# Performance work log

Measured on AMD Instinct MI355X. Metric: run time of the kernel, lower is better.

Reference implementation:

```python
import jax, jax.numpy as jnp
import numpy as np

C, DI, N, K, R = 64, 128, 16, 4, 4   # d_model, d_inner, d_state, d_conv, dt_rank
B, H, W = 4, 96, 96


def _layer_params(key):
    ks = jax.random.split(key, 6)
    p = {}
    p['ln_g'] = jnp.ones((C,), jnp.float32)
    p['ln_b'] = jnp.zeros((C,), jnp.float32)
    p['in_w'] = jax.random.normal(ks[0], (2 * DI, C), jnp.float32) / np.sqrt(C)
    p['conv_w'] = jax.random.normal(ks[1], (DI, K), jnp.float32) / np.sqrt(K)
    p['conv_b'] = jnp.zeros((DI,), jnp.float32)
    p['xp_w'] = jax.random.normal(ks[2], (R + 2 * N, DI), jnp.float32) / np.sqrt(DI)
    p['dt_w'] = jax.random.normal(ks[3], (DI, R), jnp.float32) / np.sqrt(R)
    p['dt_b'] = jnp.full((DI,), -4.0, jnp.float32)  # softplus(-4) ~ 0.018, sane dt
    p['A_log'] = jnp.broadcast_to(jnp.log(jnp.arange(1, N + 1, dtype=jnp.float32)), (DI, N)) + jnp.zeros((DI, N), jnp.float32)
    p['D'] = jnp.ones((DI,), jnp.float32)
    p['out_w'] = jax.random.normal(ks[4], (C, DI), jnp.float32) / np.sqrt(DI)
    p['skip'] = jnp.ones((1,), jnp.float32)
    p['pr_w'] = jax.random.normal(ks[5], (C, C), jnp.float32) / np.sqrt(C)
    p['pr_b'] = jnp.zeros((C,), jnp.float32)
    return p


def setup_inputs() -> dict:
    key = jax.random.key(0)
    k0, k1, k2 = jax.random.split(key, 3)
    inp = {'x': jax.random.normal(k0, (B, C, H, W), jnp.float32)}
    for i, k in ((1, k1), (2, k2)):
        for n, v in _layer_params(k).items():
            inp[f'{n}{i}'] = v
    return inp


def _silu(x):
    return x * jax.nn.sigmoid(x)


def _layer_norm(x, g, b, eps=1e-5):
    m = x.mean(-1, keepdims=True)
    v = x.var(-1, keepdims=True)
    return (x - m) * jax.lax.rsqrt(v + eps) * g + b


def _instance_norm(x, eps=1e-5):  # x: [B, C, H, W], no affine
    m = x.mean((2, 3), keepdims=True)
    v = x.var((2, 3), keepdims=True)
    return (x - m) * jax.lax.rsqrt(v + eps)


def _causal_conv(x, w, b):  # x: [B, L, D]; w: [D, K] depthwise; causal pad left
    L = x.shape[1]
    xp = jnp.pad(x, ((0, 0), (K - 1, 0), (0, 0)))
    y = b
    for k in range(K):
        y = y + xp[:, k:k + L, :] * w[:, k]
    return y


def _mamba(x, in_w, conv_w, conv_b, xp_w, dt_w, dt_b, A_log, Dp, out_w):
    # x: [B, L, C]
    xz = x @ in_w.T                       # [B, L, 2*DI]
    xin, z = jnp.split(xz, 2, axis=-1)
    xc = _silu(_causal_conv(xin, conv_w, conv_b))   # [B, L, DI]
    dbl = xc @ xp_w.T                     # [B, L, R + 2N]
    dt, Bm, Cm = jnp.split(dbl, [R, R + N], axis=-1)
    dt = jax.nn.softplus(dt @ dt_w.T + dt_b)        # [B, L, DI]
    A = -jnp.exp(A_log)                   # [DI, N]
    a = jnp.exp(dt[..., None] * A)                        # [B, L, DI, N]
    bb = dt[..., None] * Bm[:, :, None, :] * xc[..., None]  # [B, L, DI, N]

    def comb(l, r):
        a1, b1 = l
        a2, b2 = r
        return (a1 * a2, a2 * b1 + b2)

    _, h = jax.lax.associative_scan(comb, (a, bb), axis=1)  # h: [B, L, DI, N]
    y = jnp.einsum('bldn,bln->bld', h, Cm) + Dp * xc
    y = y * _silu(z)
    return y @ out_w.T                    # [B, L, C]


def _mamba_layer(x4, p):
    # x4: [B, C, H, W]
    b, c, h, w = x4.shape
    xf = x4.reshape(b, c, h * w).transpose(0, 2, 1)   # [B, L, C]
    xn = _layer_norm(xf, p['ln_g'], p['ln_b'])
    xm = _mamba(xn, p['in_w'], p['conv_w'], p['conv_b'], p['xp_w'], p['dt_w'],
                p['dt_b'], p['A_log'], p['D'], p['out_w']) + p['skip'] * xf
    xm = xm @ p['pr_w'].T + p['pr_b']
    return xm.transpose(0, 2, 1).reshape(b, c, h, w)


_PNAMES = ['ln_g', 'ln_b', 'in_w', 'conv_w', 'conv_b', 'xp_w', 'dt_w', 'dt_b',
           'A_log', 'D', 'out_w', 'skip', 'pr_w', 'pr_b']


def _forward(x, *ps):
    p1 = dict(zip(_PNAMES, ps[:14]))
    p2 = dict(zip(_PNAMES, ps[14:]))
    identity = x
    h = jax.nn.relu(_instance_norm(x))
    h = _mamba_layer(h, p1)
    h = jax.nn.relu(_instance_norm(h))
    h = _mamba_layer(h, p2)
    return h + identity


def reference(x, ln_g1, ln_b1, in_w1, conv_w1, conv_b1, xp_w1, dt_w1, dt_b1,
              A_log1, D1, out_w1, skip1, pr_w1, pr_b1,
              ln_g2, ln_b2, in_w2, conv_w2, conv_b2, xp_w2, dt_w2, dt_b2,
              A_log2, D2, out_w2, skip2, pr_w2, pr_b2):
    return _forward(x, ln_g1, ln_b1, in_w1, conv_w1, conv_b1, xp_w1, dt_w1, dt_b1,
                    A_log1, D1, out_w1, skip1, pr_w1, pr_b1,
                    ln_g2, ln_b2, in_w2, conv_w2, conv_b2, xp_w2, dt_w2, dt_b2,
                    A_log2, D2, out_w2, skip2, pr_w2, pr_b2)
```

## Files before the change

kernel.cpp:

```cpp
#include <hip/hip_runtime.h>
#include <math.h>

#define BB 4
#define CC 64
#define DI 128
#define NS 16
#define LL 9216
#define NT (LL / 64)

#define GCH 576
#define LCH 16
#define NSEQ 8192
#define SD  512
#define NG 24
#define GS 24

typedef __attribute__((ext_vector_type(8))) short bf16x8;
typedef __attribute__((ext_vector_type(4))) float fx4;
#define MFMA16 __builtin_amdgcn_mfma_f32_16x16x32_bf16

static __device__ __forceinline__ unsigned short f2b(float f) {
  unsigned u = __float_as_uint(f);
  u += 0x7fffu + ((u >> 16) & 1u);
  return (unsigned short)(u >> 16);
}
static __device__ __forceinline__ float b2f(unsigned short s) {
  return __uint_as_float(((unsigned)s) << 16);
}
static __device__ __forceinline__ float silu_f(float x) {
  return x / (1.f + __expf(-x));
}

static __device__ __forceinline__ void powers16(float e1, float* a) {
  float p2 = e1 * e1, p4 = p2 * p2, p8 = p4 * p4;
  a[0] = e1;      a[1] = p2;      a[2] = p2 * e1;      a[3] = p4;
  a[4] = p4 * e1; a[5] = p4 * p2; a[6] = p4 * p2 * e1; a[7] = p8;
  a[8] = p8 * e1; a[9] = p8 * p2; a[10] = p8 * p2 * e1; a[11] = p8 * p4;
  a[12] = p8 * p4 * e1; a[13] = p8 * p4 * p2; a[14] = p8 * p4 * p2 * e1; a[15] = p8 * p8;
}

static __device__ __forceinline__ float dt_and_a(float v, float A0, bool aone, bool afast,
                                                 const float* __restrict__ Alog, int d,
                                                 float* a) {
  float em = __expf(-fabsf(v));
  float t = 1.f + em;
  float dtv = fmaxf(v, 0.f) + __logf(t);
  if (aone) {
    float e1 = ((v >= 0.f) ? em : 1.f) / t;
    powers16(e1, a);
  } else if (afast) {
    powers16(__expf(dtv * A0), a);
  } else {
    #pragma unroll
    for (int n = 0; n < 16; ++n) a[n] = __expf(dtv * -__expf(Alog[d * NS + n]));
  }
  return dtv;
}

__global__ __launch_bounds__(256) void k_cvt(const float* __restrict__ inw1, const float* __restrict__ xpw1,
                                             const float* __restrict__ ow1, const float* __restrict__ pw1,
                                             const float* __restrict__ inw2, const float* __restrict__ xpw2,
                                             const float* __restrict__ ow2, const float* __restrict__ pw2,
                                             unsigned short* __restrict__ wb) {
  int idx = blockIdx.x * 256 + threadIdx.x;
  int layer = idx >= 34816;
  int e = idx - layer * 34816;
  const float* inw = layer ? inw2 : inw1;
  const float* xpw = layer ? xpw2 : xpw1;
  const float* ow = layer ? ow2 : ow1;
  const float* pw = layer ? pw2 : pw1;
  float v;
  if (e < 16384) v = inw[e];
  else if (e < 22528) { int t = e - 16384; int r = t >> 7, c = t & 127; v = (r < 36) ? xpw[r * 128 + c] : 0.f; }
  else if (e < 30720) v = ow[e - 22528];
  else v = pw[e - 30720];
  wb[idx] = f2b(v);
}

__global__ __launch_bounds__(256) void k_stats(const float* __restrict__ p,
                                               float* __restrict__ stats) {
  int bc = blockIdx.x;
  const float* row = p + (size_t)bc * LL;
  float s = 0.f, s2 = 0.f;
  for (int i = threadIdx.x; i < LL; i += 256) {
    float v = row[i];
    s += v; s2 += v * v;
  }
  #pragma unroll
  for (int o = 32; o > 0; o >>= 1) {
    s += __shfl_down(s, o);
    s2 += __shfl_down(s2, o);
  }
  __shared__ float red[8];
  int w = threadIdx.x >> 6;
  if ((threadIdx.x & 63) == 0) { red[w] = s; red[4 + w] = s2; }
  __syncthreads();
  if (threadIdx.x == 0) {
    float S = red[0] + red[1] + red[2] + red[3];
    float S2 = red[4] + red[5] + red[6] + red[7];
    float m = S * (1.f / LL);
    float var = S2 * (1.f / LL) - m * m;
    stats[bc * 2] = m;
    stats[bc * 2 + 1] = rsqrtf(var + 1e-5f);
  }
}

__global__ __launch_bounds__(256) void k_fusein(const float* __restrict__ p,
                                                const float* __restrict__ stats,
                                                const float* __restrict__ g,
                                                const float* __restrict__ be,
                                                const unsigned short* __restrict__ w_b,
                                                float* __restrict__ xf,
                                                unsigned short* __restrict__ xin_b,
                                                unsigned short* __restrict__ sz_b) {
  int b = blockIdx.x / NT;
  int l0 = (blockIdx.x % NT) * 64;
  __shared__ float T[64][65];
  __shared__ unsigned short Tb[64][72];
  int li = threadIdx.x & 63;
  int c0 = threadIdx.x >> 6;
  #pragma unroll
  for (int j = 0; j < 16; ++j) {
    int c = c0 * 16 + j;
    float m = stats[(b * CC + c) * 2];
    float rs = stats[(b * CC + c) * 2 + 1];
    float v = p[((size_t)(b * CC + c)) * LL + l0 + li];
    T[li][c] = fmaxf((v - m) * rs, 0.f);
  }
  __syncthreads();
  int lane = threadIdx.x & 63;
  int w = threadIdx.x >> 6;
  float gv = g[lane], bv = be[lane];
  for (int j = 0; j < 16; ++j) {
    int row = w * 16 + j;
    float v = T[row][lane];
    float s = v, s2 = v * v;
    #pragma unroll
    for (int o = 32; o > 0; o >>= 1) { s += __shfl_xor(s, o); s2 += __shfl_xor(s2, o); }
    float m = s * (1.f / 64.f);
    float var = s2 * (1.f / 64.f) - m * m;
    float rs = rsqrtf(var + 1e-5f);
    size_t off = ((size_t)b * LL + l0 + row) * CC + lane;
    xf[off] = v;
    Tb[row][lane] = f2b((v - m) * rs * gv + bv);
  }
  __syncthreads();
  int wv = threadIdx.x >> 6;
  int lr = lane & 15, kg = lane >> 4;
  int m0 = wv * 16;
  int rowg0 = blockIdx.x * 64 + m0;
  bf16x8 a0 = *(const bf16x8*)&Tb[m0 + lr][kg * 8];
  bf16x8 a1 = *(const bf16x8*)&Tb[m0 + lr][32 + kg * 8];
  #pragma unroll
  for (int nt = 0; nt < 16; ++nt) {
    bf16x8 b0 = *(const bf16x8*)&w_b[(size_t)(nt * 16 + lr) * CC + kg * 8];
    bf16x8 b1 = *(const bf16x8*)&w_b[(size_t)(nt * 16 + lr) * CC + 32 + kg * 8];
    fx4 c = {0.f, 0.f, 0.f, 0.f};
    c = MFMA16(a0, b0, c, 0, 0, 0);
    c = MFMA16(a1, b1, c, 0, 0, 0);
    #pragma unroll
    for (int r = 0; r < 4; ++r) {
      int row = rowg0 + kg * 4 + r, col = nt * 16 + lr;
      if (col < 128) xin_b[(size_t)row * DI + col] = f2b(c[r]);
      else           sz_b[(size_t)row * DI + col - 128] = f2b(silu_f(c[r]));
    }
  }
}

__global__ __launch_bounds__(128) void k_scanAX(const unsigned short* __restrict__ xin_b,
                                                const float* __restrict__ cw,
                                                const float* __restrict__ cb,
                                                const unsigned short* __restrict__ xpw_b,
                                                const float* __restrict__ Alog,
                                                const float* __restrict__ dtw,
                                                const float* __restrict__ dtbp,
                                                float* __restrict__ dbl,
                                                unsigned short* __restrict__ xc_b,
                                                float* __restrict__ dts,
                                                float* __restrict__ hl) {
  int g = blockIdx.x % GCH;
  int b = blockIdx.x / GCH;
  __shared__ float dblP[2][16][40];
  __shared__ unsigned short xcS[16][136];
  int wv = threadIdx.x >> 6, lane = threadIdx.x & 63;
  int lr = lane & 15, kg = lane >> 4;
  {
    int lloc = g * LCH + lr;
    size_t row = (size_t)b * LL + lloc;
    const bf16x8 zv8 = {0, 0, 0, 0, 0, 0, 0, 0};
    fx4 acc[3];
    #pragma unroll
    for (int nt = 0; nt < 3; ++nt) acc[nt] = (fx4){0.f, 0.f, 0.f, 0.f};
    #pragma unroll
    for (int kk = 0; kk < 2; ++kk) {
      int cbase = (wv * 2 + kk) * 32 + kg * 8;
      bf16x8 x3 = *(const bf16x8*)&xin_b[row * DI + cbase];
      bf16x8 x2 = (lloc >= 1) ? *(const bf16x8*)&xin_b[(row - 1) * DI + cbase] : zv8;
      bf16x8 x1 = (lloc >= 2) ? *(const bf16x8*)&xin_b[(row - 2) * DI + cbase] : zv8;
      bf16x8 x0 = (lloc >= 3) ? *(const bf16x8*)&xin_b[(row - 3) * DI + cbase] : zv8;
      bf16x8 a;
      #pragma unroll
      for (int e = 0; e < 8; ++e) {
        int dd = cbase + e;
        float4 w4 = *(const float4*)&cw[dd * 4];
        float v = cb[dd] + b2f((unsigned short)x0[e]) * w4.x + b2f((unsigned short)x1[e]) * w4.y
                + b2f((unsigned short)x2[e]) * w4.z + b2f((unsigned short)x3[e]) * w4.w;
        a[e] = (short)f2b(silu_f(v));
      }
      *(bf16x8*)&xcS[lr][cbase] = a;
      #pragma unroll
      for (int nt = 0; nt < 3; ++nt) {
        bf16x8 bfr = *(const bf16x8*)&xpw_b[(size_t)(nt * 16 + lr) * DI + cbase];
        acc[nt] = MFMA16(a, bfr, acc[nt], 0, 0, 0);
      }
    }
    #pragma unroll
    for (int nt = 0; nt < 3; ++nt)
      #pragma unroll
      for (int r = 0; r < 4; ++r) {
        int col = nt * 16 + lr;
        if (col < 36) dblP[wv][kg * 4 + r][col] = acc[nt][r];
      }
  }
  __syncthreads();
  {
    size_t dbase = ((size_t)b * LL + g * LCH) * 36;
    for (int e = threadIdx.x; e < 576; e += 128) {
      int r = e / 36, c = e - r * 36;
      float v = dblP[0][r][c] + dblP[1][r][c];
      dblP[0][r][c] = v;
      dbl[dbase + e] = v;
    }
    size_t xbase = ((size_t)b * LL + g * LCH) * DI;
    #pragma unroll
    for (int j = 0; j < 2; ++j) {
      int c = threadIdx.x + 128 * j;
      int row = c >> 4, col = (c & 15) * 8;
      *(bf16x8*)&xc_b[xbase + row * DI + col] = *(const bf16x8*)&xcS[row][col];
    }
  }
  __syncthreads();
  int d = threadIdx.x;
  float A0 = -__expf(Alog[d * NS]);
  bool afast = true;
  #pragma unroll
  for (int n = 1; n < 16; ++n) {
    float An = -__expf(Alog[d * NS + n]);
    afast = afast && (fabsf(An - A0 * (float)(n + 1)) <= 1e-3f * (float)(n + 1) * fabsf(A0));
  }
  bool aone = afast && (A0 == -1.0f);
  float4 w4 = *(const float4*)&dtw[d * 4];
  float dtbv = dtbp[d];
  float h[16];
  #pragma unroll
  for (int n = 0; n < 16; ++n) h[n] = 0.f;
  float dtsum = 0.f;
  #pragma unroll 4
  for (int l = 0; l < LCH; ++l) {
    float xcv = b2f(xcS[l][d]);
    float4 qv = *(float4*)&dblP[0][l][0];
    float v = dtbv + qv.x * w4.x + qv.y * w4.y + qv.z * w4.z + qv.w * w4.w;
    float a[16];
    float dtv = dt_and_a(v, A0, aone, afast, Alog, d, a);
    float dx = dtv * xcv;
    dtsum += dtv;
    float4 b0 = *(float4*)&dblP[0][l][4];
    float4 b1 = *(float4*)&dblP[0][l][8];
    float4 b2 = *(float4*)&dblP[0][l][12];
    float4 b3 = *(float4*)&dblP[0][l][16];
    h[0]  = a[0]  * h[0]  + dx * b0.x;  h[1]  = a[1]  * h[1]  + dx * b0.y;
    h[2]  = a[2]  * h[2]  + dx * b0.z;  h[3]  = a[3]  * h[3]  + dx * b0.w;
    h[4]  = a[4]  * h[4]  + dx * b1.x;  h[5]  = a[5]  * h[5]  + dx * b1.y;
    h[6]  = a[6]  * h[6]  + dx * b1.z;  h[7]  = a[7]  * h[7]  + dx * b1.w;
    h[8]  = a[8]  * h[8]  + dx * b2.x;  h[9]  = a[9]  * h[9]  + dx * b2.y;
    h[10] = a[10] * h[10] + dx * b2.z;  h[11] = a[11] * h[11] + dx * b2.w;
    h[12] = a[12] * h[12] + dx * b3.x;  h[13] = a[13] * h[13] + dx * b3.y;
    h[14] = a[14] * h[14] + dx * b3.z;  h[15] = a[15] * h[15] + dx * b3.w;
  }
  dts[(size_t)g * SD + b * DI + d] = dtsum;
  size_t o = (size_t)g * NSEQ + ((size_t)b * DI + d) * NS;
  #pragma unroll
  for (int j = 0; j < 4; ++j)
    *(float4*)&hl[o + j * 4] = make_float4(h[j * 4], h[j * 4 + 1], h[j * 4 + 2], h[j * 4 + 3]);
}

__global__ __launch_bounds__(256) void k_scan2a(const float* __restrict__ dts,
                                                const float* __restrict__ hl,
                                                const float* __restrict__ Alog,
                                                float* __restrict__ gap,
                                                float* __restrict__ ghl) {
  int t = blockIdx.x * 256 + threadIdx.x;
  int grp = t >> 13, seq = t & (NSEQ - 1);
  int sd = seq >> 4;
  float An = -__expf(Alog[seq & (DI * NS - 1)]);
  float A = 1.f, H = 0.f;
  int c0 = grp * GS;
  #pragma unroll 4
  for (int c = 0; c < GS; ++c) {
    float a = __expf(An * dts[(size_t)(c0 + c) * SD + sd]);
    H = a * H + hl[(size_t)(c0 + c) * NSEQ + seq];
    A *= a;
  }
  gap[t] = A;
  ghl[t] = H;
}

__global__ __launch_bounds__(256) void k_scan2bc(const float* __restrict__ dts,
                                                 const float* __restrict__ hl,
                                                 const float* __restrict__ gap,
                                                 const float* __restrict__ ghl,
                                                 const float* __restrict__ Alog,
                                                 float* __restrict__ hi) {
  int t = blockIdx.x * 256 + threadIdx.x;
  int grp = t >> 13, seq = t & (NSEQ - 1);
  int sd = seq >> 4;
  float An = -__expf(Alog[seq & (DI * NS - 1)]);
  float h = 0.f;
  for (int gg = 0; gg < grp; ++gg)
    h = gap[gg * NSEQ + seq] * h + ghl[gg * NSEQ + seq];
  int c0 = grp * GS;
  #pragma unroll 4
  for (int c = 0; c < GS; ++c) {
    float a = __expf(An * dts[(size_t)(c0 + c) * SD + sd]);
    hi[(size_t)(c0 + c) * NSEQ + seq] = h;
    h = a * h + hl[(size_t)(c0 + c) * NSEQ + seq];
  }
}

__global__ __launch_bounds__(128) void k_scanCO(const float* __restrict__ dbl,
                                                const unsigned short* __restrict__ xc_b,
                                                const unsigned short* __restrict__ sz_b,
                                                const float* __restrict__ Alog,
                                                const float* __restrict__ dtw,
                                                const float* __restrict__ dtbp,
                                                const float* __restrict__ Dp,
                                                const float* __restrict__ hi,
                                                const unsigned short* __restrict__ ow_b,
                                                const float* __restrict__ xf,
                                                const float* __restrict__ skipv,
                                                const unsigned short* __restrict__ pw_b,
                                                const float* __restrict__ pb,
                                                const float* __restrict__ ident,
                                                float* __restrict__ dst, int addid) {
  int g = blockIdx.x % GCH;
  int b = blockIdx.x / GCH;
  int d = threadIdx.x;
  __shared__ float Bms[LCH * NS];
  __shared__ float Cms[LCH * NS];
  __shared__ float Dts[LCH][4];
  __shared__ unsigned short xcS[16][136];
  __shared__ unsigned short yS[16][136];
  __shared__ unsigned short tmpS[16][72];
  {
    int tid = threadIdx.x;
    size_t rb0 = ((size_t)b * LL + g * LCH) * 36;
    if (tid < 64) {
      int l = tid >> 2, n4 = (tid & 3) * 4;
      *(float4*)&Bms[l * 16 + n4] = *(const float4*)&dbl[rb0 + (size_t)l * 36 + 4 + n4];
    } else {
      int l = (tid - 64) >> 2, n4 = (tid & 3) * 4;
      *(float4*)&Cms[l * 16 + n4] = *(const float4*)&dbl[rb0 + (size_t)l * 36 + 20 + n4];
    }
    if (tid < 16)
      *(float4*)&Dts[tid][0] = *(const float4*)&dbl[rb0 + (size_t)tid * 36];
    size_t xbase = ((size_t)b * LL + g * LCH) * DI;
    #pragma unroll
    for (int j = 0; j < 2; ++j) {
      int c = tid + 128 * j;
      int row = c >> 4, col = (c & 15) * 8;
      *(bf16x8*)&xcS[row][col] = *(const bf16x8*)&xc_b[xbase + row * DI + col];
    }
  }
  float A0 = -__expf(Alog[d * NS]);
  bool afast = true;
  #pragma unroll
  for (int n = 1; n < 16; ++n) {
    float An = -__expf(Alog[d * NS + n]);
    afast = afast && (fabsf(An - A0 * (float)(n + 1)) <= 1e-3f * (float)(n + 1) * fabsf(A0));
  }
  bool aone = afast && (A0 == -1.0f);
  float4 w4 = *(const float4*)&dtw[d * 4];
  float dtbv = dtbp[d];
  float Dv = Dp[d];
  __syncthreads();
  size_t o = (size_t)g * NSEQ + ((size_t)b * DI + d) * NS;
  float h[16];
  #pragma unroll
  for (int j = 0; j < 4; ++j) {
    float4 hv = *(const float4*)&hi[o + j * 4];
    h[j * 4 + 0] = hv.x; h[j * 4 + 1] = hv.y; h[j * 4 + 2] = hv.z; h[j * 4 + 3] = hv.w;
  }
  size_t base = ((size_t)b * LL + g * LCH) * DI + d;
  #pragma unroll 4
  for (int l = 0; l < LCH; ++l) {
    float xcv = b2f(xcS[l][d]);
    float sg = b2f(sz_b[base + (size_t)l * DI]);
    float4 qv = *(float4*)&Dts[l][0];
    float v = dtbv + qv.x * w4.x + qv.y * w4.y + qv.z * w4.z + qv.w * w4.w;
    float a[16];
    float dtv = dt_and_a(v, A0, aone, afast, Alog, d, a);
    float4 b0 = *(float4*)&Bms[l * 16];
    float4 b1 = *(float4*)&Bms[l * 16 + 4];
    float4 b2 = *(float4*)&Bms[l * 16 + 8];
    float4 b3 = *(float4*)&Bms[l * 16 + 12];
    float4 c0 = *(float4*)&Cms[l * 16];
    float4 c1 = *(float4*)&Cms[l * 16 + 4];
    float4 c2 = *(float4*)&Cms[l * 16 + 8];
    float4 c3 = *(float4*)&Cms[l * 16 + 12];
    float dx = dtv * xcv;
    float yv = Dv * xcv;
    h[0]  = a[0]  * h[0]  + dx * b0.x;  yv += h[0]  * c0.x;
    h[1]  = a[1]  * h[1]  + dx * b0.y;  yv += h[1]  * c0.y;
    h[2]  = a[2]  * h[2]  + dx * b0.z;  yv += h[2]  * c0.z;
    h[3]  = a[3]  * h[3]  + dx * b0.w;  yv += h[3]  * c0.w;
    h[4]  = a[4]  * h[4]  + dx * b1.x;  yv += h[4]  * c1.x;
    h[5]  = a[5]  * h[5]  + dx * b1.y;  yv += h[5]  * c1.y;
    h[6]  = a[6]  * h[6]  + dx * b1.z;  yv += h[6]  * c1.z;
    h[7]  = a[7]  * h[7]  + dx * b1.w;  yv += h[7]  * c1.w;
    h[8]  = a[8]  * h[8]  + dx * b2.x;  yv += h[8]  * c2.x;
    h[9]  = a[9]  * h[9]  + dx * b2.y;  yv += h[9]  * c2.y;
    h[10] = a[10] * h[10] + dx * b2.z;  yv += h[10] * c2.z;
    h[11] = a[11] * h[11] + dx * b2.w;  yv += h[11] * c2.w;
    h[12] = a[12] * h[12] + dx * b3.x;  yv += h[12] * c3.x;
    h[13] = a[13] * h[13] + dx * b3.y;  yv += h[13] * c3.y;
    h[14] = a[14] * h[14] + dx * b3.z;  yv += h[14] * c3.z;
    h[15] = a[15] * h[15] + dx * b3.w;  yv += h[15] * c3.w;
    yS[l][d] = f2b(yv * sg);
  }
  __syncthreads();
  int lane = threadIdx.x & 63;
  int lr = lane & 15, kg = lane >> 4;
  int lw = threadIdx.x >> 6;
  {
    fx4 oacc[2];
    oacc[0] = (fx4){0.f, 0.f, 0.f, 0.f};
    oacc[1] = (fx4){0.f, 0.f, 0.f, 0.f};
    #pragma unroll
    for (int ks = 0; ks < 4; ++ks) {
      int cbase = ks * 32 + kg * 8;
      bf16x8 a = *(const bf16x8*)&yS[lr][cbase];
      #pragma unroll
      for (int j = 0; j < 2; ++j) {
        int nt = lw * 2 + j;
        bf16x8 bfr = *(const bf16x8*)&ow_b[(size_t)(nt * 16 + lr) * DI + cbase];
        oacc[j] = MFMA16(a, bfr, oacc[j], 0, 0, 0);
      }
    }
    float sk = skipv[0];
    #pragma unroll
    for (int j = 0; j < 2; ++j) {
      int nt = lw * 2 + j;
      #pragma unroll
      for (int r = 0; r < 4; ++r) {
        int rowl = kg * 4 + r, col = nt * 16 + lr;
        size_t grow = (size_t)b * LL + g * LCH + rowl;
        tmpS[rowl][col] = f2b(oacc[j][r] + sk * xf[grow * CC + col]);
      }
    }
  }
  __syncthreads();
  {
    fx4 pacc[2];
    pacc[0] = (fx4){0.f, 0.f, 0.f, 0.f};
    pacc[1] = (fx4){0.f, 0.f, 0.f, 0.f};
    #pragma unroll
    for (int ks = 0; ks < 2; ++ks) {
      int cbase = ks * 32 + kg * 8;
      bf16x8 bfrag = *(const bf16x8*)&tmpS[lr][cbase];
      #pragma unroll
      for (int j = 0; j < 2; ++j) {
        int ct = lw * 2 + j;
        bf16x8 a = *(const bf16x8*)&pw_b[(size_t)(ct * 16 + lr) * CC + cbase];
        pacc[j] = MFMA16(a, bfrag, pacc[j], 0, 0, 0);
      }
    }
    #pragma unroll
    for (int j = 0; j < 2; ++j) {
      int ct = lw * 2 + j;
      #pragma unroll
      for (int r = 0; r < 4; ++r) {
        int c = ct * 16 + kg * 4 + r;
        int lpos = g * LCH + lr;
        size_t off = ((size_t)(b * CC + c)) * LL + lpos;
        float val = pacc[j][r] + pb[c];
        if (addid) val += ident[off];
        dst[off] = val;
      }
    }
  }
}

extern "C" void kernel_launch(void* const* d_in, const int* in_sizes, int n_in,
                              void* d_out, int out_size, void* d_ws, size_t ws_size,
                              hipStream_t stream) {
  const float* x = (const float*)d_in[0];
  float* ws = (float*)d_ws;
  float* stats = ws;
  float* xf    = ws + 1024;
  unsigned short* xin_b = (unsigned short*)(ws + 2360320);
  unsigned short* sz_b  = (unsigned short*)(ws + 4719616);
  float* dbl   = ws + 7078912;
  float* dts   = ws + 8406016;
  float* hl    = ws + 8700928;
  float* hi    = ws + 13419520;
  float* gap   = ws + 18138112;
  float* ghl   = ws + 18334720;
  unsigned short* wb = (unsigned short*)(ws + 18531328);
  unsigned short* xc_b = (unsigned short*)(ws + 18566144);
  float* inter = hl;
  float* outp  = (float*)d_out;

  k_cvt<<<272, 256, 0, stream>>>((const float*)d_in[3], (const float*)d_in[6],
                                 (const float*)d_in[11], (const float*)d_in[13],
                                 (const float*)d_in[17], (const float*)d_in[20],
                                 (const float*)d_in[25], (const float*)d_in[27], wb);

  const float* cur = x;
  for (int layer = 0; layer < 2; ++layer) {
    const int p0 = 1 + 14 * layer;
    const float* ln_g   = (const float*)d_in[p0 + 0];
    const float* ln_b   = (const float*)d_in[p0 + 1];
    const float* conv_w = (const float*)d_in[p0 + 3];
    const float* conv_b = (const float*)d_in[p0 + 4];
    const float* dt_w   = (const float*)d_in[p0 + 6];
    const float* dt_b   = (const float*)d_in[p0 + 7];
    const float* A_log  = (const float*)d_in[p0 + 8];
    const float* Dp     = (const float*)d_in[p0 + 9];
    const float* skip   = (const float*)d_in[p0 + 11];
    const float* pr_b   = (const float*)d_in[p0 + 13];
    const unsigned short* inw_b = wb + (size_t)layer * 34816;
    const unsigned short* xpw_b = inw_b + 16384;
    const unsigned short* ow_b  = inw_b + 22528;
    const unsigned short* pw_b  = inw_b + 30720;
    float* dst = (layer == 0) ? inter : outp;

    k_stats  <<<BB * CC, 256, 0, stream>>>(cur, stats);
    k_fusein <<<BB * NT, 256, 0, stream>>>(cur, stats, ln_g, ln_b, inw_b, xf, xin_b, sz_b);
    k_scanAX <<<BB * GCH, 128, 0, stream>>>(xin_b, conv_w, conv_b, xpw_b, A_log,
                                            dt_w, dt_b, dbl, xc_b, dts, hl);
    k_scan2a <<<(NG * NSEQ) / 256, 256, 0, stream>>>(dts, hl, A_log, gap, ghl);
    k_scan2bc<<<(NG * NSEQ) / 256, 256, 0, stream>>>(dts, hl, gap, ghl, A_log, hi);
    k_scanCO <<<BB * GCH, 128, 0, stream>>>(dbl, xc_b, sz_b, A_log, dt_w, dt_b, Dp,
                                            hi, ow_b, xf, skip, pw_b, pr_b, x, dst, layer);
    cur = inter;
  }
}
```

Baseline: 237.1 us.

## Split scan output into local partial and carried-state correction to avoid rescan

```diff
diff --git a/kernel.cpp b/kernel.cpp
--- a/kernel.cpp
+++ b/kernel.cpp
@@ -128,23 +128,35 @@
     T[li][c] = fmaxf((v - m) * rs, 0.f);
   }
   __syncthreads();
-  int lane = threadIdx.x & 63;
-  int w = threadIdx.x >> 6;
-  float gv = g[lane], bv = be[lane];
-  for (int j = 0; j < 16; ++j) {
-    int row = w * 16 + j;
-    float v = T[row][lane];
-    float s = v, s2 = v * v;
-    #pragma unroll
-    for (int o = 32; o > 0; o >>= 1) { s += __shfl_xor(s, o); s2 += __shfl_xor(s2, o); }
+  {
+    int row = threadIdx.x >> 2, part = threadIdx.x & 3;
+    int ch0 = part * 16;
+    float s = 0.f, s2 = 0.f;
+    #pragma unroll
+    for (int j = 0; j < 16; ++j) {
+      float v = T[row][ch0 + j];
+      s += v; s2 += v * v;
+    }
+    s += __shfl_xor(s, 1); s2 += __shfl_xor(s2, 1);
+    s += __shfl_xor(s, 2); s2 += __shfl_xor(s2, 2);
     float m = s * (1.f / 64.f);
     float var = s2 * (1.f / 64.f) - m * m;
     float rs = rsqrtf(var + 1e-5f);
-    size_t off = ((size_t)b * LL + l0 + row) * CC + lane;
-    xf[off] = v;
-    Tb[row][lane] = f2b((v - m) * rs * gv + bv);
-  }
-  __syncthreads();
+    size_t off0 = ((size_t)b * LL + l0 + row) * CC + ch0;
+    #pragma unroll
+    for (int j4 = 0; j4 < 4; ++j4) {
+      float4 v4 = *(float4*)&T[row][ch0 + j4 * 4];
+      *(float4*)&xf[off0 + j4 * 4] = v4;
+      float4 g4 = *(const float4*)&g[ch0 + j4 * 4];
+      float4 b4 = *(const float4*)&be[ch0 + j4 * 4];
+      Tb[row][ch0 + j4 * 4 + 0] = f2b((v4.x - m) * rs * g4.x + b4.x);
+      Tb[row][ch0 + j4 * 4 + 1] = f2b((v4.y - m) * rs * g4.y + b4.y);
+      Tb[row][ch0 + j4 * 4 + 2] = f2b((v4.z - m) * rs * g4.z + b4.z);
+      Tb[row][ch0 + j4 * 4 + 3] = f2b((v4.w - m) * rs * g4.w + b4.w);
+    }
+  }
+  __syncthreads();
+  int lane = threadIdx.x & 63;
   int wv = threadIdx.x >> 6;
   int lr = lane & 15, kg = lane >> 4;
   int m0 = wv * 16;
@@ -174,10 +186,12 @@
                                                 const float* __restrict__ Alog,
                                                 const float* __restrict__ dtw,
                                                 const float* __restrict__ dtbp,
-                                                float* __restrict__ dbl,
+                                                float* __restrict__ dblC,
                                                 unsigned short* __restrict__ xc_b,
                                                 float* __restrict__ dts,
-                                                float* __restrict__ hl) {
+                                                float* __restrict__ hl,
+                                                float* __restrict__ y1G,
+                                                float* __restrict__ dtpreG) {
   int g = blockIdx.x % GCH;
   int b = blockIdx.x / GCH;
   __shared__ float dblP[2][16][40];
@@ -224,12 +238,18 @@
   }
   __syncthreads();
   {
-    size_t dbase = ((size_t)b * LL + g * LCH) * 36;
     for (int e = threadIdx.x; e < 576; e += 128) {
       int r = e / 36, c = e - r * 36;
-      float v = dblP[0][r][c] + dblP[1][r][c];
-      dblP[0][r][c] = v;
-      dbl[dbase + e] = v;
+      dblP[0][r][c] += dblP[1][r][c];
+    }
+  }
+  __syncthreads();
+  {
+    size_t cbase16 = ((size_t)b * LL + g * LCH) * 16;
+    #pragma unroll
+    for (int j = 0; j < 2; ++j) {
+      int e = threadIdx.x + 128 * j;
+      dblC[cbase16 + e] = dblP[0][e >> 4][20 + (e & 15)];
     }
     size_t xbase = ((size_t)b * LL + g * LCH) * DI;
     #pragma unroll
@@ -239,7 +259,6 @@
       *(bf16x8*)&xc_b[xbase + row * DI + col] = *(const bf16x8*)&xcS[row][col];
     }
   }
-  __syncthreads();
   int d = threadIdx.x;
   float A0 = -__expf(Alog[d * NS]);
   bool afast = true;
@@ -255,6 +274,7 @@
   #pragma unroll
   for (int n = 0; n < 16; ++n) h[n] = 0.f;
   float dtsum = 0.f;
+  size_t sbase = ((size_t)b * LL + g * LCH) * DI + d;
   #pragma unroll 4
   for (int l = 0; l < LCH; ++l) {
     float xcv = b2f(xcS[l][d]);
@@ -276,6 +296,16 @@
     h[10] = a[10] * h[10] + dx * b2.z;  h[11] = a[11] * h[11] + dx * b2.w;
     h[12] = a[12] * h[12] + dx * b3.x;  h[13] = a[13] * h[13] + dx * b3.y;
     h[14] = a[14] * h[14] + dx * b3.z;  h[15] = a[15] * h[15] + dx * b3.w;
+    float4 cc0 = *(float4*)&dblP[0][l][20];
+    float4 cc1 = *(float4*)&dblP[0][l][24];
+    float4 cc2 = *(float4*)&dblP[0][l][28];
+    float4 cc3 = *(float4*)&dblP[0][l][32];
+    float y0 = h[0] * cc0.x + h[1] * cc0.y + h[2] * cc0.z + h[3] * cc0.w;
+    float y1 = h[4] * cc1.x + h[5] * cc1.y + h[6] * cc1.z + h[7] * cc1.w;
+    float y2 = h[8] * cc2.x + h[9] * cc2.y + h[10] * cc2.z + h[11] * cc2.w;
+    float y3 = h[12] * cc3.x + h[13] * cc3.y + h[14] * cc3.z + h[15] * cc3.w;
+    y1G[sbase + (size_t)l * DI] = (y0 + y1) + (y2 + y3);
+    dtpreG[sbase + (size_t)l * DI] = dtsum;
   }
   dts[(size_t)g * SD + b * DI + d] = dtsum;
   size_t o = (size_t)g * NSEQ + ((size_t)b * DI + d) * NS;
@@ -327,12 +357,12 @@
   }
 }
 
-__global__ __launch_bounds__(128) void k_scanCO(const float* __restrict__ dbl,
+__global__ __launch_bounds__(128) void k_scanCO(const float* __restrict__ dblC,
                                                 const unsigned short* __restrict__ xc_b,
                                                 const unsigned short* __restrict__ sz_b,
+                                                const float* __restrict__ y1G,
+                                                const float* __restrict__ dtpreG,
                                                 const float* __restrict__ Alog,
-                                                const float* __restrict__ dtw,
-                                                const float* __restrict__ dtbp,
                                                 const float* __restrict__ Dp,
                                                 const float* __restrict__ hi,
                                                 const unsigned short* __restrict__ ow_b,
@@ -345,24 +375,14 @@
   int g = blockIdx.x % GCH;
   int b = blockIdx.x / GCH;
   int d = threadIdx.x;
-  __shared__ float Bms[LCH * NS];
   __shared__ float Cms[LCH * NS];
-  __shared__ float Dts[LCH][4];
   __shared__ unsigned short xcS[16][136];
   __shared__ unsigned short yS[16][136];
   __shared__ unsigned short tmpS[16][72];
   {
     int tid = threadIdx.x;
-    size_t rb0 = ((size_t)b * LL + g * LCH) * 36;
-    if (tid < 64) {
-      int l = tid >> 2, n4 = (tid & 3) * 4;
-      *(float4*)&Bms[l * 16 + n4] = *(const float4*)&dbl[rb0 + (size_t)l * 36 + 4 + n4];
-    } else {
-      int l = (tid - 64) >> 2, n4 = (tid & 3) * 4;
-      *(float4*)&Cms[l * 16 + n4] = *(const float4*)&dbl[rb0 + (size_t)l * 36 + 20 + n4];
-    }
-    if (tid < 16)
-      *(float4*)&Dts[tid][0] = *(const float4*)&dbl[rb0 + (size_t)tid * 36];
+    size_t cb16 = ((size_t)b * LL + g * LCH) * 16;
+    if (tid < 64) *(float4*)&Cms[tid * 4] = *(const float4*)&dblC[cb16 + tid * 4];
     size_t xbase = ((size_t)b * LL + g * LCH) * DI;
     #pragma unroll
     for (int j = 0; j < 2; ++j) {
@@ -378,53 +398,38 @@
     float An = -__expf(Alog[d * NS + n]);
     afast = afast && (fabsf(An - A0 * (float)(n + 1)) <= 1e-3f * (float)(n + 1) * fabsf(A0));
   }
-  bool aone = afast && (A0 == -1.0f);
-  float4 w4 = *(const float4*)&dtw[d * 4];
-  float dtbv = dtbp[d];
   float Dv = Dp[d];
   __syncthreads();
   size_t o = (size_t)g * NSEQ + ((size_t)b * DI + d) * NS;
-  float h[16];
+  float hiR[16];
   #pragma unroll
   for (int j = 0; j < 4; ++j) {
     float4 hv = *(const float4*)&hi[o + j * 4];
-    h[j * 4 + 0] = hv.x; h[j * 4 + 1] = hv.y; h[j * 4 + 2] = hv.z; h[j * 4 + 3] = hv.w;
+    hiR[j * 4 + 0] = hv.x; hiR[j * 4 + 1] = hv.y; hiR[j * 4 + 2] = hv.z; hiR[j * 4 + 3] = hv.w;
   }
   size_t base = ((size_t)b * LL + g * LCH) * DI + d;
   #pragma unroll 4
   for (int l = 0; l < LCH; ++l) {
+    float dtpre = dtpreG[base + (size_t)l * DI];
+    float y1v = y1G[base + (size_t)l * DI];
     float xcv = b2f(xcS[l][d]);
     float sg = b2f(sz_b[base + (size_t)l * DI]);
-    float4 qv = *(float4*)&Dts[l][0];
-    float v = dtbv + qv.x * w4.x + qv.y * w4.y + qv.z * w4.z + qv.w * w4.w;
-    float a[16];
-    float dtv = dt_and_a(v, A0, aone, afast, Alog, d, a);
-    float4 b0 = *(float4*)&Bms[l * 16];
-    float4 b1 = *(float4*)&Bms[l * 16 + 4];
-    float4 b2 = *(float4*)&Bms[l * 16 + 8];
-    float4 b3 = *(float4*)&Bms[l * 16 + 12];
+    float pw[16];
+    if (afast) {
+      powers16(__expf(A0 * dtpre), pw);
+    } else {
+      #pragma unroll
+      for (int n = 0; n < 16; ++n) pw[n] = __expf(-__expf(Alog[d * NS + n]) * dtpre);
+    }
     float4 c0 = *(float4*)&Cms[l * 16];
     float4 c1 = *(float4*)&Cms[l * 16 + 4];
     float4 c2 = *(float4*)&Cms[l * 16 + 8];
     float4 c3 = *(float4*)&Cms[l * 16 + 12];
-    float dx = dtv * xcv;
-    float yv = Dv * xcv;
-    h[0]  = a[0]  * h[0]  + dx * b0.x;  yv += h[0]  * c0.x;
-    h[1]  = a[1]  * h[1]  + dx * b0.y;  yv += h[1]  * c0.y;
-    h[2]  = a[2]  * h[2]  + dx * b0.z;  yv += h[2]  * c0.z;
-    h[3]  = a[3]  * h[3]  + dx * b0.w;  yv += h[3]  * c0.w;
-    h[4]  = a[4]  * h[4]  + dx * b1.x;  yv += h[4]  * c1.x;
-    h[5]  = a[5]  * h[5]  + dx * b1.y;  yv += h[5]  * c1.y;
-    h[6]  = a[6]  * h[6]  + dx * b1.z;  yv += h[6]  * c1.z;
-    h[7]  = a[7]  * h[7]  + dx * b1.w;  yv += h[7]  * c1.w;
-    h[8]  = a[8]  * h[8]  + dx * b2.x;  yv += h[8]  * c2.x;
-    h[9]  = a[9]  * h[9]  + dx * b2.y;  yv += h[9]  * c2.y;
-    h[10] = a[10] * h[10] + dx * b2.z;  yv += h[10] * c2.z;
-    h[11] = a[11] * h[11] + dx * b2.w;  yv += h[11] * c2.w;
-    h[12] = a[12] * h[12] + dx * b3.x;  yv += h[12] * c3.x;
-    h[13] = a[13] * h[13] + dx * b3.y;  yv += h[13] * c3.y;
-    h[14] = a[14] * h[14] + dx * b3.z;  yv += h[14] * c3.z;
-    h[15] = a[15] * h[15] + dx * b3.w;  yv += h[15] * c3.w;
+    float s0 = c0.x * pw[0] * hiR[0] + c0.y * pw[1] * hiR[1] + c0.z * pw[2] * hiR[2] + c0.w * pw[3] * hiR[3];
+    float s1 = c1.x * pw[4] * hiR[4] + c1.y * pw[5] * hiR[5] + c1.z * pw[6] * hiR[6] + c1.w * pw[7] * hiR[7];
+    float s2 = c2.x * pw[8] * hiR[8] + c2.y * pw[9] * hiR[9] + c2.z * pw[10] * hiR[10] + c2.w * pw[11] * hiR[11];
+    float s3 = c3.x * pw[12] * hiR[12] + c3.y * pw[13] * hiR[13] + c3.z * pw[14] * hiR[14] + c3.w * pw[15] * hiR[15];
+    float yv = y1v + Dv * xcv + ((s0 + s1) + (s2 + s3));
     yS[l][d] = f2b(yv * sg);
   }
   __syncthreads();
@@ -499,14 +504,16 @@
   float* xf    = ws + 1024;
   unsigned short* xin_b = (unsigned short*)(ws + 2360320);
   unsigned short* sz_b  = (unsigned short*)(ws + 4719616);
-  float* dbl   = ws + 7078912;
-  float* dts   = ws + 8406016;
-  float* hl    = ws + 8700928;
-  float* hi    = ws + 13419520;
-  float* gap   = ws + 18138112;
-  float* ghl   = ws + 18334720;
-  unsigned short* wb = (unsigned short*)(ws + 18531328);
-  unsigned short* xc_b = (unsigned short*)(ws + 18566144);
+  float* dblC  = ws + 7078912;
+  float* dts   = ws + 7668736;
+  float* hl    = ws + 7963648;
+  float* hi    = ws + 12682240;
+  float* gap   = ws + 17400832;
+  float* ghl   = ws + 17597440;
+  unsigned short* wb = (unsigned short*)(ws + 17794048);
+  unsigned short* xc_b = (unsigned short*)(ws + 17828864);
+  float* y1G   = ws + 20188160;
+  float* dtpreG = ws + 24906752;
   float* inter = hl;
   float* outp  = (float*)d_out;
 
@@ -537,10 +544,10 @@
     k_stats  <<<BB * CC, 256, 0, stream>>>(cur, stats);
     k_fusein <<<BB * NT, 256, 0, stream>>>(cur, stats, ln_g, ln_b, inw_b, xf, xin_b, sz_b);
     k_scanAX <<<BB * GCH, 128, 0, stream>>>(xin_b, conv_w, conv_b, xpw_b, A_log,
-                                            dt_w, dt_b, dbl, xc_b, dts, hl);
+                                            dt_w, dt_b, dblC, xc_b, dts, hl, y1G, dtpreG);
     k_scan2a <<<(NG * NSEQ) / 256, 256, 0, stream>>>(dts, hl, A_log, gap, ghl);
     k_scan2bc<<<(NG * NSEQ) / 256, 256, 0, stream>>>(dts, hl, gap, ghl, A_log, hi);
-    k_scanCO <<<BB * GCH, 128, 0, stream>>>(dbl, xc_b, sz_b, A_log, dt_w, dt_b, Dp,
+    k_scanCO <<<BB * GCH, 128, 0, stream>>>(dblC, xc_b, sz_b, y1G, dtpreG, A_log, Dp,
                                             hi, ow_b, xf, skip, pw_b, pr_b, x, dst, layer);
     cur = inter;
   }
```

Measured after the change: 230.8 us. 1.03x faster.
